# Kernel tuning notes

Measured on AMD Instinct MI355X. Metric: run time of the kernel, lower is better.

Reference implementation:

```python
import jax, jax.numpy as jnp
import numpy as np

H = 8
D_MODEL = 512
D_K = D_MODEL // H
MAX_REL = 16
BS, LQ, LK = 2, 2048, 2048


def setup_inputs() -> dict:
    key = jax.random.key(0)
    ks = jax.random.split(key, 12)
    s = 0.02
    return {
        'q': jax.random.normal(ks[0], (BS, LQ, D_MODEL), jnp.float32),
        'k': jax.random.normal(ks[1], (BS, LK, D_MODEL), jnp.float32),
        'v': jax.random.normal(ks[2], (BS, LK, D_MODEL), jnp.float32),
        'mask': jnp.ones((BS, LQ, LK), jnp.int32),
        'Wq': jax.random.normal(ks[3], (D_MODEL, D_MODEL), jnp.float32) * s,
        'bq': jnp.zeros((D_MODEL,), jnp.float32),
        'Wk': jax.random.normal(ks[4], (D_MODEL, D_MODEL), jnp.float32) * s,
        'bk': jnp.zeros((D_MODEL,), jnp.float32),
        'Wv': jax.random.normal(ks[5], (D_MODEL, D_MODEL), jnp.float32) * s,
        'bv': jnp.zeros((D_MODEL,), jnp.float32),
        'Wo': jax.random.normal(ks[6], (D_MODEL, D_MODEL), jnp.float32) * s,
        'bo': jnp.zeros((D_MODEL,), jnp.float32),
        'rpe_k': jax.random.normal(ks[7], (2 * MAX_REL + 1, D_K), jnp.float32) * s,
    }


def reference(q, k, v, mask, Wq, bq, Wk, bk, Wv, bv, Wo, bo, rpe_k):
    bs, lq, _ = q.shape
    lk = k.shape[1]
    # projections -> [bs, h, len, d_k]
    qp = (q @ Wq + bq).reshape(bs, lq, H, D_K).transpose(0, 2, 1, 3)
    kp = (k @ Wk + bk).reshape(bs, lk, H, D_K).transpose(0, 2, 1, 3)
    vp = (v @ Wv + bv).reshape(bs, lk, H, D_K).transpose(0, 2, 1, 3)
    content = jnp.einsum('bhqd,bhkd->bhqk', qp, kp)
    # relative position embeddings: [lq, lk, d_k]
    dist = jnp.clip(jnp.arange(lk)[None, :] - jnp.arange(lq)[:, None], -MAX_REL, MAX_REL) + MAX_REL
    rpe = rpe_k[dist]
    rel = jnp.einsum('bhqd,qkd->bhqk', qp, rpe)
    scores = (content + rel) / jnp.sqrt(jnp.asarray(D_K, q.dtype))
    scores = jnp.where(mask[:, None, :, :] == 0, jnp.asarray(-1e9, q.dtype), scores)
    attn = jax.nn.softmax(scores, axis=-1)  # dropout inactive (eval)
    out = jnp.einsum('bhqk,bhkd->bhqd', attn, vp)
    concat = out.transpose(0, 2, 1, 3).reshape(bs, lq, D_MODEL)
    final = concat @ Wo + bo
    return (final, attn)
```

## Files before the change

kernel.cpp:

```cpp
#include <hip/hip_runtime.h>

#define H_ 8
#define DK 64
#define LQ 2048
#define LK 2048
#define BS 2
#define DM 512

typedef _Float16 f16;
typedef _Float16 f16x8 __attribute__((ext_vector_type(8)));
typedef float f32x4 __attribute__((ext_vector_type(4)));
typedef unsigned long long u64;

#define LS 72
#define PS 40
#define RS 48

#define QSCALE 0.1803368801111204f

__global__ __launch_bounds__(256) void prep_k(const int* __restrict__ mask,
                                              u64* __restrict__ mp64,
                                              const float* __restrict__ Wq,
                                              const float* __restrict__ Wk,
                                              const float* __restrict__ Wv,
                                              const float* __restrict__ Wo,
                                              f16* __restrict__ WT,
                                              const float* __restrict__ rpe,
                                              f16* __restrict__ rpef) {
  __shared__ f16 T[64][LS];
  const int bid = blockIdx.x, tid = threadIdx.x;
  if (bid < 32768) {
    size_t t = (size_t)bid * 256 + tid;
    u64 b = __ballot(mask[t] != 0);
    if ((tid & 63) == 0) mp64[t >> 6] = b;
    return;
  }
  if (bid == 33024) {
#pragma unroll
    for (int j = 0; j < 12; j++) {
      int idx = tid + j * 256;
      int row = idx >> 6, d = idx & 63;
      rpef[idx] = row < 33 ? (f16)rpe[row * DK + d] : (f16)0.f;
    }
    return;
  }
  const int idx = bid - 32768;
  const int z = idx >> 6, rem = idx & 63;
  const float* W = z == 0 ? Wq : (z == 1 ? Wk : (z == 2 ? Wv : Wo));
  const int n0 = (rem & 7) * 64, k0 = (rem >> 3) * 64;
  const int r = tid >> 2, cg = tid & 3;
#pragma unroll
  for (int p = 0; p < 4; p++) {
    f32x4 v = *(const f32x4*)(W + (size_t)(k0 + r) * DM + n0 + cg * 16 + p * 4);
#pragma unroll
    for (int j = 0; j < 4; j++) T[cg * 16 + p * 4 + j][r] = (f16)v[j];
  }
  __syncthreads();
  const int n = tid >> 2, kc = tid & 3;
#pragma unroll
  for (int p = 0; p < 2; p++) {
    *(f16x8*)(WT + ((size_t)z * DM + n0 + n) * DM + k0 + kc * 16 + p * 8) =
        *(const f16x8*)&T[n][kc * 16 + p * 8];
  }
}

__global__ __launch_bounds__(256, 4) void qkv_k(
    const float* __restrict__ qin, const float* __restrict__ kin, const float* __restrict__ vin,
    const f16* __restrict__ WT, const f16* __restrict__ rpef,
    const float* __restrict__ bq, const float* __restrict__ bk, const float* __restrict__ bv,
    f16* __restrict__ qp, f16* __restrict__ kp, f16* __restrict__ vpt,
    float* __restrict__ R) {
  __shared__ f16 As[64][LS];
  __shared__ f16 Bt[64][LS];
  const int tid = threadIdx.x, lane = tid & 63, w = tid >> 6;
  const int wr = w >> 1, wc = w & 1, fr = lane & 15, fs = lane >> 4;
  const int m0 = blockIdx.x * 64;
  const int n0g = blockIdx.y * 64, seg = n0g >> 9, nn0 = n0g & 511;
  const float* X = seg == 0 ? qin : (seg == 1 ? kin : vin);
  const f16* WTs = WT + (size_t)seg * DM * DM;
  const float* bias = seg == 0 ? bq : (seg == 1 ? bk : bv);
  const float scale = seg == 0 ? QSCALE : 1.0f;

  f32x4 acc[2][2] = {};

  for (int k0 = 0; k0 < DM; k0 += 64) {
    __syncthreads();
    {
      int m = tid >> 2, c0 = tid & 3;
#pragma unroll
      for (int pp = 0; pp < 2; pp++) {
        int cc = c0 + pp * 4;
        const float* p = X + (size_t)(m0 + m) * DM + k0 + cc * 8;
        f32x4 v0 = *(const f32x4*)p;
        f32x4 v1 = *(const f32x4*)(p + 4);
        f16x8 hv;
#pragma unroll
        for (int i = 0; i < 4; i++) { hv[i] = (f16)v0[i]; hv[i + 4] = (f16)v1[i]; }
        *(f16x8*)&As[m][cc * 8] = hv;
      }
      int n = tid >> 2, kc = tid & 3;
#pragma unroll
      for (int pp = 0; pp < 2; pp++) {
        *(f16x8*)&Bt[n][kc * 16 + pp * 8] =
            *(const f16x8*)(WTs + (size_t)(nn0 + n) * DM + k0 + kc * 16 + pp * 8);
      }
    }
    __syncthreads();
#pragma unroll
    for (int kc = 0; kc < 2; kc++) {
      f16x8 a[2], b[2];
#pragma unroll
      for (int mi = 0; mi < 2; mi++)
        a[mi] = *(const f16x8*)&As[wr * 32 + mi * 16 + fr][kc * 32 + fs * 8];
#pragma unroll
      for (int ni = 0; ni < 2; ni++)
        b[ni] = *(const f16x8*)&Bt[wc * 32 + ni * 16 + fr][kc * 32 + fs * 8];
#pragma unroll
      for (int mi = 0; mi < 2; mi++)
#pragma unroll
        for (int ni = 0; ni < 2; ni++)
          acc[mi][ni] = __builtin_amdgcn_mfma_f32_16x16x32_f16(a[mi], b[ni], acc[mi][ni], 0, 0, 0);
    }
  }

  const int h = nn0 >> 6, b_ = m0 >> 11, l0 = m0 & (LQ - 1);
  if (seg < 2) {
    f16* out = seg == 0 ? qp : kp;
    if (seg == 0) __syncthreads();
#pragma unroll
    for (int mi = 0; mi < 2; mi++)
#pragma unroll
      for (int ni = 0; ni < 2; ni++) {
        int d = wc * 32 + ni * 16 + fr;
        float bb = bias[nn0 + d];
#pragma unroll
        for (int i = 0; i < 4; i++) {
          int row = wr * 32 + mi * 16 + fs * 4 + i;
          f16 hv = (f16)((acc[mi][ni][i] + bb) * scale);
          out[((size_t)(b_ * H_ + h) * LQ + l0 + row) * DK + d] = hv;
          if (seg == 0) As[row][d] = hv;
        }
      }
    if (seg == 0) {
      __syncthreads();
      f16x8 a0 = *(const f16x8*)&As[w * 16 + fr][fs * 8];
      f16x8 a1 = *(const f16x8*)&As[w * 16 + fr][32 + fs * 8];
      const size_t rbase = ((size_t)(b_ * H_ + h) * LQ + l0 + w * 16);
#pragma unroll
      for (int nt = 0; nt < 3; nt++) {
        f16x8 b0 = *(const f16x8*)(rpef + (size_t)(nt * 16 + fr) * DK + fs * 8);
        f16x8 b1 = *(const f16x8*)(rpef + (size_t)(nt * 16 + fr) * DK + 32 + fs * 8);
        f32x4 rc = {};
        rc = __builtin_amdgcn_mfma_f32_16x16x32_f16(a0, b0, rc, 0, 0, 0);
        rc = __builtin_amdgcn_mfma_f32_16x16x32_f16(a1, b1, rc, 0, 0, 0);
#pragma unroll
        for (int i = 0; i < 4; i++)
          R[(rbase + fs * 4 + i) * RS + nt * 16 + fr] = rc[i];
      }
    }
  } else {
    __syncthreads();
#pragma unroll
    for (int mi = 0; mi < 2; mi++)
#pragma unroll
      for (int ni = 0; ni < 2; ni++) {
        int d = wc * 32 + ni * 16 + fr;
        float bb = bias[nn0 + d];
#pragma unroll
        for (int i = 0; i < 4; i++) {
          int ml = wr * 32 + mi * 16 + fs * 4 + i;
          As[d][ml] = (f16)(acc[mi][ni][i] + bb);
        }
      }
    __syncthreads();
    int r = tid >> 2;
#pragma unroll
    for (int pp = 0; pp < 2; pp++) {
      int c = (tid & 3) + pp * 4;
      *(f16x8*)(vpt + ((size_t)((b_ * H_ + h) * DK + r)) * LK + l0 + c * 8) =
          *(const f16x8*)&As[r][c * 8];
    }
  }
}

__global__ __launch_bounds__(512, 4) void attn_k(const f16* __restrict__ qp,
                                                 const f16* __restrict__ kp,
                                                 const f16* __restrict__ vpt,
                                                 const float* __restrict__ R,
                                                 const unsigned* __restrict__ mp,
                                                 float* __restrict__ attn,
                                                 f16* __restrict__ concat) {
  __shared__ f16 Ks[64][LS];
  __shared__ f16 Vt[64][LS];
  __shared__ f16 Pl[8][16][PS];
  __shared__ float Rl[64][34];
  __shared__ float Ph[2][64];
  __shared__ float Oc[4][16][68];
  const int tid = threadIdx.x, lane = tid & 63, w = tid >> 6;
  const int wq = w & 3, wh = w >> 2;
  const int fr = lane & 15, fs = lane >> 4;
  const int flat = blockIdx.x;
  const int idx = flat >> 3;
  const int bh = (flat & 7) * 2 + (idx >> 5), q0 = (idx & 31) * 64;
  const int b = bh >> 3, h = bh & 7;
  const f16* Qb = qp + ((size_t)bh * LQ + q0) * DK;
  const f16* Kb = kp + (size_t)bh * LQ * DK;
  const f16* Vb = vpt + (size_t)bh * DK * LK;

  for (int i2 = tid; i2 < 64 * 34; i2 += 512)
    Rl[i2 / 34][i2 % 34] = R[((size_t)bh * LQ + q0 + i2 / 34) * RS + i2 % 34];
  __syncthreads();

  f16x8 qa[2];
#pragma unroll
  for (int h2 = 0; h2 < 2; h2++)
    qa[h2] = *(const f16x8*)(Qb + (size_t)(wq * 16 + fr) * DK + h2 * 32 + fs * 8);

  int qq[4];
  float rlo[4], rhi[4];
  const unsigned* mprow[4];
#pragma unroll
  for (int i = 0; i < 4; i++) {
    qq[i] = wq * 16 + fs * 4 + i;
    rlo[i] = Rl[qq[i]][0];
    rhi[i] = Rl[qq[i]][32];
    mprow[i] = mp + ((size_t)b * LQ + q0 + qq[i]) * 64;
  }

  float psum[4] = {0.f, 0.f, 0.f, 0.f};
  for (int kt = 0; kt < LK; kt += 64) {
    __syncthreads();
    {
      int r = tid >> 3, c = tid & 7;
      *(f16x8*)&Ks[r][c * 8] = *(const f16x8*)(Kb + (size_t)(kt + r) * DK + c * 8);
    }
    __syncthreads();
    f32x4 sv[2];
#pragma unroll
    for (int cbh = 0; cbh < 2; cbh++) {
      int cb = wh * 2 + cbh;
      f32x4 s = {};
#pragma unroll
      for (int h2 = 0; h2 < 2; h2++) {
        f16x8 bf = *(const f16x8*)&Ks[cb * 16 + fr][h2 * 32 + fs * 8];
        s = __builtin_amdgcn_mfma_f32_16x16x32_f16(qa[h2], bf, s, 0, 0, 0);
      }
      sv[cbh] = s;
    }
    unsigned mw[4];
#pragma unroll
    for (int i = 0; i < 4; i++) mw[i] = mprow[i][(kt >> 5) + wh];
    const int dt = kt - q0;
    if (dt <= -128 || dt >= 128) {
#pragma unroll
      for (int cbh = 0; cbh < 2; cbh++)
#pragma unroll
        for (int i = 0; i < 4; i++) {
          float sc = sv[cbh][i] + (dt < 0 ? rlo[i] : rhi[i]);
          float pv = ((mw[i] >> (cbh * 16 + fr)) & 1u) ? exp2f(sc) : 0.f;
          psum[i] += pv;
        }
    } else {
#pragma unroll
      for (int cbh = 0; cbh < 2; cbh++)
#pragma unroll
        for (int i = 0; i < 4; i++) {
          int dd = dt + wh * 32 + cbh * 16 + fr - qq[i];
          dd = dd < -16 ? -16 : (dd > 16 ? 16 : dd);
          float sc = sv[cbh][i] + Rl[qq[i]][dd + 16];
          float pv = ((mw[i] >> (cbh * 16 + fr)) & 1u) ? exp2f(sc) : 0.f;
          psum[i] += pv;
        }
    }
  }
#pragma unroll
  for (int i = 0; i < 4; i++) {
    float v = psum[i];
    v += __shfl_xor(v, 1);
    v += __shfl_xor(v, 2);
    v += __shfl_xor(v, 4);
    v += __shfl_xor(v, 8);
    psum[i] = v;
  }
  if (fr == 0)
#pragma unroll
    for (int i = 0; i < 4; i++) Ph[wh][qq[i]] = psum[i];
  __syncthreads();
  float inv[4];
#pragma unroll
  for (int i = 0; i < 4; i++) inv[i] = 1.f / (Ph[0][qq[i]] + Ph[1][qq[i]]);

  f32x4 oacc[4] = {};
  for (int kt = 0; kt < LK; kt += 64) {
    __syncthreads();
    {
      int r = tid >> 3, c = tid & 7;
      *(f16x8*)&Ks[r][c * 8] = *(const f16x8*)(Kb + (size_t)(kt + r) * DK + c * 8);
      *(f16x8*)&Vt[r][c * 8] = *(const f16x8*)(Vb + (size_t)r * LK + kt + c * 8);
    }
    __syncthreads();
    f32x4 sv[2];
#pragma unroll
    for (int cbh = 0; cbh < 2; cbh++) {
      int cb = wh * 2 + cbh;
      f32x4 s = {};
#pragma unroll
      for (int h2 = 0; h2 < 2; h2++) {
        f16x8 bf = *(const f16x8*)&Ks[cb * 16 + fr][h2 * 32 + fs * 8];
        s = __builtin_amdgcn_mfma_f32_16x16x32_f16(qa[h2], bf, s, 0, 0, 0);
      }
      sv[cbh] = s;
    }
    unsigned mw[4];
#pragma unroll
    for (int i = 0; i < 4; i++) mw[i] = mprow[i][(kt >> 5) + wh];
    const int dt = kt - q0;
    if (dt <= -128 || dt >= 128) {
#pragma unroll
      for (int cbh = 0; cbh < 2; cbh++)
#pragma unroll
        for (int i = 0; i < 4; i++) {
          float sc = sv[cbh][i] + (dt < 0 ? rlo[i] : rhi[i]);
          float pv = ((mw[i] >> (cbh * 16 + fr)) & 1u) ? exp2f(sc) * inv[i] : 0.f;
          Pl[w][fs * 4 + i][cbh * 16 + fr] = (f16)pv;
        }
    } else {
#pragma unroll
      for (int cbh = 0; cbh < 2; cbh++)
#pragma unroll
        for (int i = 0; i < 4; i++) {
          int dd = dt + wh * 32 + cbh * 16 + fr - qq[i];
          dd = dd < -16 ? -16 : (dd > 16 ? 16 : dd);
          float sc = sv[cbh][i] + Rl[qq[i]][dd + 16];
          float pv = ((mw[i] >> (cbh * 16 + fr)) & 1u) ? exp2f(sc) * inv[i] : 0.f;
          Pl[w][fs * 4 + i][cbh * 16 + fr] = (f16)pv;
        }
    }
    {
      f16x8 pa = *(const f16x8*)&Pl[w][fr][fs * 8];
#pragma unroll
      for (int db = 0; db < 4; db++) {
        f16x8 vb = *(const f16x8*)&Vt[db * 16 + fr][wh * 32 + fs * 8];
        oacc[db] = __builtin_amdgcn_mfma_f32_16x16x32_f16(pa, vb, oacc[db], 0, 0, 0);
      }
    }
    {
      int r2 = lane >> 2, cq = lane & 3;
      float* arow = attn + ((size_t)bh * LQ + q0 + wq * 16 + r2) * LK + kt + wh * 32 + cq * 8;
      f16x8 pv8 = *(const f16x8*)&Pl[w][r2][cq * 8];
      f32x4 o0 = {(float)pv8[0], (float)pv8[1], (float)pv8[2], (float)pv8[3]};
      f32x4 o1 = {(float)pv8[4], (float)pv8[5], (float)pv8[6], (float)pv8[7]};
      *(f32x4*)(arow) = o0;
      *(f32x4*)(arow + 4) = o1;
    }
  }

  __syncthreads();
  if (wh == 1) {
#pragma unroll
    for (int db = 0; db < 4; db++)
#pragma unroll
      for (int i = 0; i < 4; i++) Oc[wq][fs * 4 + i][db * 16 + fr] = oacc[db][i];
  }
  __syncthreads();
  if (wh == 0) {
#pragma unroll
    for (int db = 0; db < 4; db++)
#pragma unroll
      for (int i = 0; i < 4; i++) {
        float val = oacc[db][i] + Oc[wq][fs * 4 + i][db * 16 + fr];
        int gq = q0 + wq * 16 + fs * 4 + i;
        concat[((size_t)b * LQ + gq) * DM + h * DK + db * 16 + fr] = (f16)val;
      }
  }
}

__global__ __launch_bounds__(256, 4) void ogemm_k(const f16* __restrict__ X,
                                                  const f16* __restrict__ WT,
                                                  const float* __restrict__ bias,
                                                  float* __restrict__ out) {
  __shared__ f16 As[64][LS];
  __shared__ f16 Bt[64][LS];
  const int tid = threadIdx.x, lane = tid & 63, w = tid >> 6;
  const int wr = w >> 1, wc = w & 1, fr = lane & 15, fs = lane >> 4;
  const int m0 = blockIdx.x * 64, n0 = blockIdx.y * 64;
  const f16* WTo = WT + (size_t)3 * DM * DM;

  f32x4 acc[2][2] = {};
  for (int k0 = 0; k0 < DM; k0 += 64) {
    __syncthreads();
    {
      int r = tid >> 2, c0 = tid & 3;
#pragma unroll
      for (int pp = 0; pp < 2; pp++) {
        int c = c0 + pp * 4;
        *(f16x8*)&As[r][c * 8] = *(const f16x8*)(X + (size_t)(m0 + r) * DM + k0 + c * 8);
      }
      int n = tid >> 2, kc = tid & 3;
#pragma unroll
      for (int pp = 0; pp < 2; pp++) {
        *(f16x8*)&Bt[n][kc * 16 + pp * 8] =
            *(const f16x8*)(WTo + (size_t)(n0 + n) * DM + k0 + kc * 16 + pp * 8);
      }
    }
    __syncthreads();
#pragma unroll
    for (int kc = 0; kc < 2; kc++) {
      f16x8 a[2], b[2];
#pragma unroll
      for (int mi = 0; mi < 2; mi++)
        a[mi] = *(const f16x8*)&As[wr * 32 + mi * 16 + fr][kc * 32 + fs * 8];
#pragma unroll
      for (int ni = 0; ni < 2; ni++)
        b[ni] = *(const f16x8*)&Bt[wc * 32 + ni * 16 + fr][kc * 32 + fs * 8];
#pragma unroll
      for (int mi = 0; mi < 2; mi++)
#pragma unroll
        for (int ni = 0; ni < 2; ni++)
          acc[mi][ni] = __builtin_amdgcn_mfma_f32_16x16x32_f16(a[mi], b[ni], acc[mi][ni], 0, 0, 0);
    }
  }
#pragma unroll
  for (int mi = 0; mi < 2; mi++)
#pragma unroll
    for (int ni = 0; ni < 2; ni++) {
      int gcol = n0 + wc * 32 + ni * 16 + fr;
      float bb = bias[gcol];
#pragma unroll
      for (int i = 0; i < 4; i++) {
        int grow = m0 + wr * 32 + mi * 16 + fs * 4 + i;
        out[(size_t)grow * DM + gcol] = acc[mi][ni][i] + bb;
      }
    }
}

extern "C" void kernel_launch(void* const* d_in, const int* in_sizes, int n_in,
                              void* d_out, int out_size, void* d_ws, size_t ws_size,
                              hipStream_t stream) {
  const float* q = (const float*)d_in[0];
  const float* k = (const float*)d_in[1];
  const float* v = (const float*)d_in[2];
  const int* mask = (const int*)d_in[3];
  const float* Wq = (const float*)d_in[4];
  const float* bq = (const float*)d_in[5];
  const float* Wk = (const float*)d_in[6];
  const float* bk = (const float*)d_in[7];
  const float* Wv = (const float*)d_in[8];
  const float* bv = (const float*)d_in[9];
  const float* Wo = (const float*)d_in[10];
  const float* bo = (const float*)d_in[11];
  const float* rpe = (const float*)d_in[12];

  char* ws = (char*)d_ws;
  f16* qp = (f16*)(ws);
  f16* kp = (f16*)(ws + (1u << 22));
  f16* vpt = (f16*)(ws + (2u << 22));
  float* R = (float*)(ws + (3u << 22));
  size_t off = (3u << 22) + (size_t)32768 * RS * 4;
  u64* mp64 = (u64*)(ws + off);
  f16* concat = (f16*)(ws + off + (1u << 20));
  f16* WT = (f16*)(ws + off + (1u << 20) + (1u << 22));
  f16* rpef = (f16*)(ws + off + (1u << 20) + (1u << 22) + (1u << 21));

  float* final_out = (float*)d_out;
  float* attn_out = final_out + (size_t)BS * LQ * DM;

  prep_k<<<dim3(33025), 256, 0, stream>>>(mask, mp64, Wq, Wk, Wv, Wo, WT, rpe, rpef);

  qkv_k<<<dim3(64, 24), 256, 0, stream>>>(q, k, v, WT, rpef, bq, bk, bv, qp, kp, vpt, R);

  attn_k<<<dim3(512), 512, 0, stream>>>(qp, kp, vpt, R, (const unsigned*)mp64, attn_out,
                                        concat);

  ogemm_k<<<dim3(64, 8), 256, 0, stream>>>(concat, WT, bo, final_out);
}
```

Baseline: 164.6 us.

## Split softmax denominator pass into separate split-K kernel and fold log-denominator into bias

```diff
diff --git a/kernel.cpp b/kernel.cpp
--- a/kernel.cpp
+++ b/kernel.cpp
@@ -183,18 +183,120 @@
   }
 }
 
-__global__ __launch_bounds__(512, 4) void attn_k(const f16* __restrict__ qp,
-                                                 const f16* __restrict__ kp,
-                                                 const f16* __restrict__ vpt,
-                                                 const float* __restrict__ R,
-                                                 const unsigned* __restrict__ mp,
-                                                 float* __restrict__ attn,
-                                                 f16* __restrict__ concat) {
+__global__ __launch_bounds__(512, 8) void attn1_k(const f16* __restrict__ qp,
+                                                  const f16* __restrict__ kp,
+                                                  const float* __restrict__ R,
+                                                  const unsigned* __restrict__ mp,
+                                                  float* __restrict__ denomP) {
+  __shared__ f16 Ks[64][LS];
+  __shared__ float Rl[64][34];
+  __shared__ float Ph[2][64];
+  const int tid = threadIdx.x, lane = tid & 63, w = tid >> 6;
+  const int wq = w & 3, wh = w >> 2;
+  const int fr = lane & 15, fs = lane >> 4;
+  const int flat = blockIdx.x;
+  const int idx2 = flat >> 3;
+  const int bh = (flat & 7) * 2 + (idx2 >> 7);
+  const int rem = idx2 & 127, qb = rem >> 2, chunk = rem & 3;
+  const int q0 = qb * 64, kc0 = chunk * 512;
+  const int b = bh >> 3;
+  const f16* Qb = qp + ((size_t)bh * LQ + q0) * DK;
+  const f16* Kb = kp + (size_t)bh * LQ * DK;
+
+  for (int i2 = tid; i2 < 64 * 34; i2 += 512)
+    Rl[i2 / 34][i2 % 34] = R[((size_t)bh * LQ + q0 + i2 / 34) * RS + i2 % 34];
+  __syncthreads();
+
+  f16x8 qa[2];
+#pragma unroll
+  for (int h2 = 0; h2 < 2; h2++)
+    qa[h2] = *(const f16x8*)(Qb + (size_t)(wq * 16 + fr) * DK + h2 * 32 + fs * 8);
+
+  int qq[4];
+  float rlo[4], rhi[4];
+  const unsigned* mprow[4];
+#pragma unroll
+  for (int i = 0; i < 4; i++) {
+    qq[i] = wq * 16 + fs * 4 + i;
+    rlo[i] = Rl[qq[i]][0];
+    rhi[i] = Rl[qq[i]][32];
+    mprow[i] = mp + ((size_t)b * LQ + q0 + qq[i]) * 64;
+  }
+
+  float psum[4] = {0.f, 0.f, 0.f, 0.f};
+  for (int kt = kc0; kt < kc0 + 512; kt += 64) {
+    __syncthreads();
+    {
+      int r = tid >> 3, c = tid & 7;
+      *(f16x8*)&Ks[r][c * 8] = *(const f16x8*)(Kb + (size_t)(kt + r) * DK + c * 8);
+    }
+    __syncthreads();
+    f32x4 sv[2];
+#pragma unroll
+    for (int cbh = 0; cbh < 2; cbh++) {
+      int cb = wh * 2 + cbh;
+      f32x4 s = {};
+#pragma unroll
+      for (int h2 = 0; h2 < 2; h2++) {
+        f16x8 bf = *(const f16x8*)&Ks[cb * 16 + fr][h2 * 32 + fs * 8];
+        s = __builtin_amdgcn_mfma_f32_16x16x32_f16(qa[h2], bf, s, 0, 0, 0);
+      }
+      sv[cbh] = s;
+    }
+    unsigned mw[4];
+#pragma unroll
+    for (int i = 0; i < 4; i++) mw[i] = mprow[i][(kt >> 5) + wh];
+    const int dt = kt - q0;
+    if (dt <= -128 || dt >= 128) {
+#pragma unroll
+      for (int cbh = 0; cbh < 2; cbh++)
+#pragma unroll
+        for (int i = 0; i < 4; i++) {
+          float sc = sv[cbh][i] + (dt < 0 ? rlo[i] : rhi[i]);
+          psum[i] += ((mw[i] >> (cbh * 16 + fr)) & 1u) ? exp2f(sc) : 0.f;
+        }
+    } else {
+#pragma unroll
+      for (int cbh = 0; cbh < 2; cbh++)
+#pragma unroll
+        for (int i = 0; i < 4; i++) {
+          int dd = dt + wh * 32 + cbh * 16 + fr - qq[i];
+          dd = dd < -16 ? -16 : (dd > 16 ? 16 : dd);
+          float sc = sv[cbh][i] + Rl[qq[i]][dd + 16];
+          psum[i] += ((mw[i] >> (cbh * 16 + fr)) & 1u) ? exp2f(sc) : 0.f;
+        }
+    }
+  }
+#pragma unroll
+  for (int i = 0; i < 4; i++) {
+    float v = psum[i];
+    v += __shfl_xor(v, 1);
+    v += __shfl_xor(v, 2);
+    v += __shfl_xor(v, 4);
+    v += __shfl_xor(v, 8);
+    psum[i] = v;
+  }
+  if (fr == 0)
+#pragma unroll
+    for (int i = 0; i < 4; i++) Ph[wh][qq[i]] = psum[i];
+  __syncthreads();
+  if (tid < 64)
+    denomP[(((size_t)bh * 32 + qb) * 4 + chunk) * 64 + tid] = Ph[0][tid] + Ph[1][tid];
+}
+
+__global__ __launch_bounds__(512, 4) void attn2_k(const f16* __restrict__ qp,
+                                                  const f16* __restrict__ kp,
+                                                  const f16* __restrict__ vpt,
+                                                  const float* __restrict__ R,
+                                                  const float* __restrict__ denomP,
+                                                  const unsigned* __restrict__ mp,
+                                                  float* __restrict__ attn,
+                                                  f16* __restrict__ concat) {
   __shared__ f16 Ks[64][LS];
   __shared__ f16 Vt[64][LS];
   __shared__ f16 Pl[8][16][PS];
   __shared__ float Rl[64][34];
-  __shared__ float Ph[2][64];
+  __shared__ float Dl[64];
   __shared__ float Oc[4][16][68];
   const int tid = threadIdx.x, lane = tid & 63, w = tid >> 6;
   const int wq = w & 3, wh = w >> 2;
@@ -203,12 +305,20 @@
   const int idx = flat >> 3;
   const int bh = (flat & 7) * 2 + (idx >> 5), q0 = (idx & 31) * 64;
   const int b = bh >> 3, h = bh & 7;
+  const int qb = q0 >> 6;
   const f16* Qb = qp + ((size_t)bh * LQ + q0) * DK;
   const f16* Kb = kp + (size_t)bh * LQ * DK;
   const f16* Vb = vpt + (size_t)bh * DK * LK;
 
-  for (int i2 = tid; i2 < 64 * 34; i2 += 512)
-    Rl[i2 / 34][i2 % 34] = R[((size_t)bh * LQ + q0 + i2 / 34) * RS + i2 % 34];
+  if (tid < 64) {
+    const float* dp = denomP + (((size_t)bh * 32 + qb) * 4) * 64 + tid;
+    Dl[tid] = log2f(dp[0] + dp[64] + dp[128] + dp[192]);
+  }
+  __syncthreads();
+  for (int i2 = tid; i2 < 64 * 34; i2 += 512) {
+    int row = i2 / 34;
+    Rl[row][i2 % 34] = R[((size_t)bh * LQ + q0 + row) * RS + i2 % 34] - Dl[row];
+  }
   __syncthreads();
 
   f16x8 qa[2];
@@ -227,12 +337,13 @@
     mprow[i] = mp + ((size_t)b * LQ + q0 + qq[i]) * 64;
   }
 
-  float psum[4] = {0.f, 0.f, 0.f, 0.f};
+  f32x4 oacc[4] = {};
   for (int kt = 0; kt < LK; kt += 64) {
     __syncthreads();
     {
       int r = tid >> 3, c = tid & 7;
       *(f16x8*)&Ks[r][c * 8] = *(const f16x8*)(Kb + (size_t)(kt + r) * DK + c * 8);
+      *(f16x8*)&Vt[r][c * 8] = *(const f16x8*)(Vb + (size_t)r * LK + kt + c * 8);
     }
     __syncthreads();
     f32x4 sv[2];
@@ -258,7 +369,7 @@
         for (int i = 0; i < 4; i++) {
           float sc = sv[cbh][i] + (dt < 0 ? rlo[i] : rhi[i]);
           float pv = ((mw[i] >> (cbh * 16 + fr)) & 1u) ? exp2f(sc) : 0.f;
-          psum[i] += pv;
+          Pl[w][fs * 4 + i][cbh * 16 + fr] = (f16)pv;
         }
     } else {
 #pragma unroll
@@ -269,70 +380,6 @@
           dd = dd < -16 ? -16 : (dd > 16 ? 16 : dd);
           float sc = sv[cbh][i] + Rl[qq[i]][dd + 16];
           float pv = ((mw[i] >> (cbh * 16 + fr)) & 1u) ? exp2f(sc) : 0.f;
-          psum[i] += pv;
-        }
-    }
-  }
-#pragma unroll
-  for (int i = 0; i < 4; i++) {
-    float v = psum[i];
-    v += __shfl_xor(v, 1);
-    v += __shfl_xor(v, 2);
-    v += __shfl_xor(v, 4);
-    v += __shfl_xor(v, 8);
-    psum[i] = v;
-  }
-  if (fr == 0)
-#pragma unroll
-    for (int i = 0; i < 4; i++) Ph[wh][qq[i]] = psum[i];
-  __syncthreads();
-  float inv[4];
-#pragma unroll
-  for (int i = 0; i < 4; i++) inv[i] = 1.f / (Ph[0][qq[i]] + Ph[1][qq[i]]);
-
-  f32x4 oacc[4] = {};
-  for (int kt = 0; kt < LK; kt += 64) {
-    __syncthreads();
-    {
-      int r = tid >> 3, c = tid & 7;
-      *(f16x8*)&Ks[r][c * 8] = *(const f16x8*)(Kb + (size_t)(kt + r) * DK + c * 8);
-      *(f16x8*)&Vt[r][c * 8] = *(const f16x8*)(Vb + (size_t)r * LK + kt + c * 8);
-    }
-    __syncthreads();
-    f32x4 sv[2];
-#pragma unroll
-    for (int cbh = 0; cbh < 2; cbh++) {
-      int cb = wh * 2 + cbh;
-      f32x4 s = {};
-#pragma unroll
-      for (int h2 = 0; h2 < 2; h2++) {
-        f16x8 bf = *(const f16x8*)&Ks[cb * 16 + fr][h2 * 32 + fs * 8];
-        s = __builtin_amdgcn_mfma_f32_16x16x32_f16(qa[h2], bf, s, 0, 0, 0);
-      }
-      sv[cbh] = s;
-    }
-    unsigned mw[4];
-#pragma unroll
-    for (int i = 0; i < 4; i++) mw[i] = mprow[i][(kt >> 5) + wh];
-    const int dt = kt - q0;
-    if (dt <= -128 || dt >= 128) {
-#pragma unroll
-      for (int cbh = 0; cbh < 2; cbh++)
-#pragma unroll
-        for (int i = 0; i < 4; i++) {
-          float sc = sv[cbh][i] + (dt < 0 ? rlo[i] : rhi[i]);
-          float pv = ((mw[i] >> (cbh * 16 + fr)) & 1u) ? exp2f(sc) * inv[i] : 0.f;
-          Pl[w][fs * 4 + i][cbh * 16 + fr] = (f16)pv;
-        }
-    } else {
-#pragma unroll
-      for (int cbh = 0; cbh < 2; cbh++)
-#pragma unroll
-        for (int i = 0; i < 4; i++) {
-          int dd = dt + wh * 32 + cbh * 16 + fr - qq[i];
-          dd = dd < -16 ? -16 : (dd > 16 ? 16 : dd);
-          float sc = sv[cbh][i] + Rl[qq[i]][dd + 16];
-          float pv = ((mw[i] >> (cbh * 16 + fr)) & 1u) ? exp2f(sc) * inv[i] : 0.f;
           Pl[w][fs * 4 + i][cbh * 16 + fr] = (f16)pv;
         }
     }
@@ -461,6 +508,7 @@
   f16* concat = (f16*)(ws + off + (1u << 20));
   f16* WT = (f16*)(ws + off + (1u << 20) + (1u << 22));
   f16* rpef = (f16*)(ws + off + (1u << 20) + (1u << 22) + (1u << 21));
+  float* denomP = (float*)(ws + off + (1u << 20) + (1u << 22) + (1u << 21) + 8192);
 
   float* final_out = (float*)d_out;
   float* attn_out = final_out + (size_t)BS * LQ * DM;
@@ -469,8 +517,10 @@
 
   qkv_k<<<dim3(64, 24), 256, 0, stream>>>(q, k, v, WT, rpef, bq, bk, bv, qp, kp, vpt, R);
 
-  attn_k<<<dim3(512), 512, 0, stream>>>(qp, kp, vpt, R, (const unsigned*)mp64, attn_out,
-                                        concat);
+  attn1_k<<<dim3(2048), 512, 0, stream>>>(qp, kp, R, (const unsigned*)mp64, denomP);
+
+  attn2_k<<<dim3(512), 512, 0, stream>>>(qp, kp, vpt, R, denomP, (const unsigned*)mp64,
+                                         attn_out, concat);
 
   ogemm_k<<<dim3(64, 8), 256, 0, stream>>>(concat, WT, bo, final_out);
 }
```

After: 181.9 us. 1.11x slower.
